# Kernel optimization log

Hardware: AMD Instinct MI355X
Metric: run time of the kernel (lower is better)

## Reference

```python
import jax, jax.numpy as jnp
import numpy as np


def setup_inputs() -> dict:
    key = jax.random.key(0)
    k1, k2, k3, k4 = jax.random.split(key, 4)
    B, S, d_in, d_out = 4, 2048, 1024, 1024
    x = jax.random.normal(k1, (B, S, d_in), dtype=jnp.float32)
    # torch nn.Linear weight is [d_out, d_in]; we store transposed [d_in, d_out]
    Wq = jax.random.normal(k2, (d_in, d_out), dtype=jnp.float32) * (1.0 / np.sqrt(d_in))
    Wk = jax.random.normal(k3, (d_in, d_out), dtype=jnp.float32) * (1.0 / np.sqrt(d_in))
    Wv = jax.random.normal(k4, (d_in, d_out), dtype=jnp.float32) * (1.0 / np.sqrt(d_in))
    return {"x": x, "Wq": Wq, "Wk": Wk, "Wv": Wv}


def reference(x, Wq, Wk, Wv):
    # x: [B, S, d_in]
    B, S, d_in = x.shape
    q = jnp.einsum("bsd,de->bse", x, Wq)
    k = jnp.einsum("bsd,de->bse", x, Wk)
    v = jnp.einsum("bsd,de->bse", x, Wv)
    scores = jnp.einsum("bqe,bke->bqk", q, k)  # [B, S, S]
    causal = jnp.triu(jnp.ones((S, S), dtype=bool), k=1)  # True above diagonal
    scores = jnp.where(causal[None, :, :], -jnp.inf, scores)
    # NOTE: original scales by sqrt(d_in), not sqrt(d_out)
    scale = jnp.asarray(1.0 / np.sqrt(d_in), dtype=scores.dtype)
    weights = jax.nn.softmax(scores * scale, axis=-1)
    # dropout p=0.0 -> identity
    return jnp.einsum("bqk,bke->bqe", weights, v)
```

## Files before the change

kernel.cpp:

```cpp
#include <hip/hip_runtime.h>
#include <hip/hip_bf16.h>

typedef __attribute__((ext_vector_type(8))) short short8;
typedef __attribute__((ext_vector_type(4))) float f32x4;
typedef unsigned short ushort_t;

__device__ __forceinline__ ushort_t f2bf(float f) {
    union { __hip_bfloat16 h; ushort_t u; } c;
    c.h = __float2bfloat16(f);
    return c.u;
}

__device__ __forceinline__ void gload16(const ushort_t* g, ushort_t* l) {
    __builtin_amdgcn_global_load_lds(
        (const __attribute__((address_space(1))) void*)g,
        (__attribute__((address_space(3))) void*)l, 16, 0, 0);
}

__global__ __launch_bounds__(256) void k_prep(const float* __restrict__ x,
                                              const float* __restrict__ W0,
                                              const float* __restrict__ W1,
                                              const float* __restrict__ W2,
                                              ushort_t* __restrict__ xb,
                                              ushort_t* __restrict__ Wt) {
    const int bz = blockIdx.z;
    if (bz == 3) {
        const int t = threadIdx.y * 32 + threadIdx.x;
        size_t base = ((size_t)(blockIdx.y * 32 + blockIdx.x) * 256 + t) * 8;
#pragma unroll
        for (int p = 0; p < 4; ++p) {
            size_t idx = base + (size_t)p * 2097152;
            float4 a = *(const float4*)(x + idx);
            float4 b = *(const float4*)(x + idx + 4);
            short8 o;
            o[0] = (short)f2bf(a.x); o[1] = (short)f2bf(a.y);
            o[2] = (short)f2bf(a.z); o[3] = (short)f2bf(a.w);
            o[4] = (short)f2bf(b.x); o[5] = (short)f2bf(b.y);
            o[6] = (short)f2bf(b.z); o[7] = (short)f2bf(b.w);
            *(short8*)(xb + idx) = o;
        }
        return;
    }
    const float* W = (bz == 0) ? W0 : (bz == 1) ? W1 : W2;
    ushort_t* out = Wt + (size_t)bz * 1024 * 1024;
    __shared__ float tile[32][33];
    int tx = threadIdx.x, ty = threadIdx.y;
    int d0 = blockIdx.y * 32, e0 = blockIdx.x * 32;
#pragma unroll
    for (int i = 0; i < 32; i += 8)
        tile[ty + i][tx] = W[(size_t)(d0 + ty + i) * 1024 + e0 + tx];
    __syncthreads();
#pragma unroll
    for (int i = 0; i < 32; i += 8)
        out[(size_t)(e0 + ty + i) * 1024 + d0 + tx] = f2bf(tile[tx][ty + i]);
}

template <int MODE>
__global__ __launch_bounds__(256) void k_gemm(const ushort_t* __restrict__ Abase,
                                              const ushort_t* __restrict__ Bbase,
                                              void* __restrict__ Cbase,
                                              ushort_t* __restrict__ Vt) {
    const int bz = blockIdx.z;
    int bm, bn;
    const ushort_t* A;
    const ushort_t* B;
    int lda, ldb, nk;
    if constexpr (MODE == 0) {
        bm = blockIdx.x; bn = blockIdx.y;
        A = Abase; lda = 1024;
        B = Bbase + (size_t)bz * 1024 * 1024; ldb = 1024;
        nk = 32;
    } else if constexpr (MODE == 1) {
        int x = blockIdx.x;
        bm = (int)((sqrtf(8.f * x + 1.f) - 1.f) * 0.5f);
        while ((bm + 1) * (bm + 2) / 2 <= x) ++bm;
        while (bm * (bm + 1) / 2 > x) --bm;
        bn = x - bm * (bm + 1) / 2;
        A = Abase + (size_t)bz * 2048 * 1024; lda = 1024;
        B = Bbase + (size_t)bz * 2048 * 1024; ldb = 1024;
        nk = 32;
    } else {
        int xr = blockIdx.x;
        bm = (xr & 1) ? (15 - (xr >> 1)) : (xr >> 1);
        bn = blockIdx.y;
        A = Abase + (size_t)bz * 2048 * 2048; lda = 2048;
        B = Bbase + (size_t)bz * 1024 * 2048; ldb = 2048;
        nk = (bm + 1) * 4;
    }

    constexpr int SMEM_ELEMS = (MODE == 0) ? (128 * 130) : 8192;
    __shared__ ushort_t smem[SMEM_ELEMS];
    ushort_t* As = smem;
    ushort_t* Bs = smem + 4096;

    const int tid = threadIdx.x;
    const int l = tid & 63, wid = tid >> 6;
    const int wr = (wid >> 1) * 64, wc = (wid & 1) * 64;
    const int lr = l & 15, kc = (l >> 4) * 8;

    const int srow = tid >> 2, skb = (tid & 3) * 8;
    const ushort_t* ag = A + (size_t)(bm * 128 + srow) * lda + skb;
    const ushort_t* bg = B + (size_t)(bn * 128 + srow) * ldb + skb;
    const size_t a64 = (size_t)64 * lda, b64 = (size_t)64 * ldb;
    ushort_t* al = As + tid * 8;
    ushort_t* bl = Bs + tid * 8;

    f32x4 zero = {0.f, 0.f, 0.f, 0.f};
    f32x4 acc[4][4];
#pragma unroll
    for (int m = 0; m < 4; ++m)
#pragma unroll
        for (int n = 0; n < 4; ++n) acc[m][n] = zero;

    f32x4 rs[4];
    short8 ones;
#pragma unroll
    for (int e = 0; e < 8; ++e) ones[e] = (short)0x3F80;
#pragma unroll
    for (int m = 0; m < 4; ++m) rs[m] = zero;

    for (int ks = 0; ks < nk; ++ks) {
        __syncthreads();
        gload16(ag, al);
        gload16(ag + a64, al + 2048);
        gload16(bg, bl);
        gload16(bg + b64, bl + 2048);
        ag += 32; bg += 32;
        __syncthreads();

        short8 a[4], b[4];
#pragma unroll
        for (int m = 0; m < 4; ++m)
            a[m] = *(const short8*)&As[(wr + m * 16 + lr) * 32 + kc];
#pragma unroll
        for (int n = 0; n < 4; ++n)
            b[n] = *(const short8*)&Bs[(wc + n * 16 + lr) * 32 + kc];
#pragma unroll
        for (int m = 0; m < 4; ++m)
#pragma unroll
            for (int n = 0; n < 4; ++n)
                acc[m][n] = __builtin_amdgcn_mfma_f32_16x16x32_bf16(a[m], b[n], acc[m][n], 0, 0, 0);
        if constexpr (MODE == 2) {
#pragma unroll
            for (int m = 0; m < 4; ++m)
                rs[m] = __builtin_amdgcn_mfma_f32_16x16x32_bf16(a[m], ones, rs[m], 0, 0, 0);
        }
    }

    const int rbase = (l >> 4) * 4;
    const int cbase = l & 15;

    if constexpr (MODE == 0) {
        if (bz == 2) {
            __syncthreads();
#pragma unroll
            for (int m = 0; m < 4; ++m)
#pragma unroll
                for (int n = 0; n < 4; ++n) {
                    int col = wc + n * 16 + cbase;
                    int row0 = wr + m * 16 + rbase;
#pragma unroll
                    for (int r = 0; r < 4; ++r)
                        smem[col * 130 + row0 + r] = f2bf(acc[m][n][r]);
                }
            __syncthreads();
            const int e = tid >> 1, jh = (tid & 1) * 64;
            const int b = bm >> 4, j0 = (bm * 128) & 2047;
            ushort_t* dst = Vt + (size_t)b * 2097152 +
                            (size_t)(bn * 128 + e) * 2048 + j0 + jh;
            const ushort_t* src = smem + e * 130 + jh;
#pragma unroll
            for (int c = 0; c < 8; ++c)
                *(short8*)(dst + c * 8) = *(const short8*)(src + c * 8);
            return;
        }
    }

    float inv[4][4];
    if constexpr (MODE == 2) {
#pragma unroll
        for (int m = 0; m < 4; ++m)
#pragma unroll
            for (int r = 0; r < 4; ++r) inv[m][r] = 1.0f / rs[m][r];
    }

#pragma unroll
    for (int m = 0; m < 4; ++m) {
#pragma unroll
        for (int n = 0; n < 4; ++n) {
            int row0 = wr + m * 16 + rbase;
            int col = wc + n * 16 + cbase;
            int gcol = bn * 128 + col;
#pragma unroll
            for (int r = 0; r < 4; ++r) {
                int grow = bm * 128 + row0 + r;
                float v = acc[m][n][r];
                if constexpr (MODE == 0) {
                    ushort_t* C = (ushort_t*)Cbase + (size_t)bz * 8192 * 1024;
                    C[(size_t)grow * 1024 + gcol] = f2bf(v);
                } else if constexpr (MODE == 1) {
                    ushort_t* C = (ushort_t*)Cbase + (size_t)bz * 2048 * 2048;
                    ushort_t pv = (gcol <= grow) ? f2bf(__expf(v * 0.03125f))
                                                 : (ushort_t)0;
                    C[(size_t)grow * 2048 + gcol] = pv;
                } else {
                    float* C = (float*)Cbase + (size_t)bz * 2048 * 1024;
                    C[(size_t)grow * 1024 + gcol] = v * inv[m][r];
                }
            }
        }
    }
}

extern "C" void kernel_launch(void* const* d_in, const int* in_sizes, int n_in,
                              void* d_out, int out_size, void* d_ws, size_t ws_size,
                              hipStream_t stream) {
    const float* x  = (const float*)d_in[0];
    const float* Wq = (const float*)d_in[1];
    const float* Wk = (const float*)d_in[2];
    const float* Wv = (const float*)d_in[3];

    char* ws = (char*)d_ws;
    ushort_t* xb     = (ushort_t*)(ws);
    ushort_t* Wt     = (ushort_t*)(ws + 16777216);
    ushort_t* QKV    = (ushort_t*)(ws + 23068672);
    ushort_t* Vt     = (ushort_t*)(ws + 73400320);
    ushort_t* P      = (ushort_t*)(ws + 90177536);

    ushort_t* Q = QKV;
    ushort_t* K = QKV + (size_t)8192 * 1024;

    k_prep<<<dim3(32, 32, 4), dim3(32, 8), 0, stream>>>(x, Wq, Wk, Wv, xb, Wt);
    k_gemm<0><<<dim3(64, 8, 3), 256, 0, stream>>>(xb, Wt, QKV, Vt);
    k_gemm<1><<<dim3(136, 1, 4), 256, 0, stream>>>(Q, K, P, nullptr);
    k_gemm<2><<<dim3(16, 8, 4), 256, 0, stream>>>(P, Vt, (float*)d_out, nullptr);
}
```

Baseline: 173.9 us.

## Fold Wq·Wk^T into one matrix so scores become x·M·x^T

Since q·k^T equals x·(Wq·Wk^T)·x^T, the change precomputes a 1024x1024 matrix M = Wk·Wq^T with a small GEMM. It then forms y = x·M and computes scores as y·x^T, instead of building separate Q and K projections. This drops one of the three large 8192x1024x1024 projection GEMMs in exchange for one 1024^3 GEMM. It also removes the K buffer and changes the weight prep to a plain cast for Wq and Wk. Rounding M and y to bf16 changes the numerical error profile slightly.

```diff
diff --git a/kernel.cpp b/kernel.cpp
--- a/kernel.cpp
+++ b/kernel.cpp
@@ -2,6 +2,7 @@
 #include <hip/hip_bf16.h>
 
 typedef __attribute__((ext_vector_type(8))) short short8;
+typedef __attribute__((ext_vector_type(4))) short short4_t;
 typedef __attribute__((ext_vector_type(4))) float f32x4;
 typedef unsigned short ushort_t;
 
@@ -18,14 +19,16 @@
 }
 
 __global__ __launch_bounds__(256) void k_prep(const float* __restrict__ x,
-                                              const float* __restrict__ W0,
-                                              const float* __restrict__ W1,
-                                              const float* __restrict__ W2,
+                                              const float* __restrict__ Wq,
+                                              const float* __restrict__ Wk,
+                                              const float* __restrict__ Wv,
                                               ushort_t* __restrict__ xb,
-                                              ushort_t* __restrict__ Wt) {
+                                              ushort_t* __restrict__ Wqb,
+                                              ushort_t* __restrict__ Wkb,
+                                              ushort_t* __restrict__ Wvt) {
     const int bz = blockIdx.z;
+    const int t = threadIdx.y * 32 + threadIdx.x;
     if (bz == 3) {
-        const int t = threadIdx.y * 32 + threadIdx.x;
         size_t base = ((size_t)(blockIdx.y * 32 + blockIdx.x) * 256 + t) * 8;
 #pragma unroll
         for (int p = 0; p < 4; ++p) {
@@ -41,18 +44,27 @@
         }
         return;
     }
-    const float* W = (bz == 0) ? W0 : (bz == 1) ? W1 : W2;
-    ushort_t* out = Wt + (size_t)bz * 1024 * 1024;
+    if (bz < 2) {
+        const float* src = bz ? Wk : Wq;
+        ushort_t* dst = bz ? Wkb : Wqb;
+        size_t idx = ((size_t)(blockIdx.y * 32 + blockIdx.x) * 256 + t) * 4;
+        float4 a = *(const float4*)(src + idx);
+        short4_t o;
+        o[0] = (short)f2bf(a.x); o[1] = (short)f2bf(a.y);
+        o[2] = (short)f2bf(a.z); o[3] = (short)f2bf(a.w);
+        *(short4_t*)(dst + idx) = o;
+        return;
+    }
     __shared__ float tile[32][33];
     int tx = threadIdx.x, ty = threadIdx.y;
     int d0 = blockIdx.y * 32, e0 = blockIdx.x * 32;
 #pragma unroll
     for (int i = 0; i < 32; i += 8)
-        tile[ty + i][tx] = W[(size_t)(d0 + ty + i) * 1024 + e0 + tx];
+        tile[ty + i][tx] = Wv[(size_t)(d0 + ty + i) * 1024 + e0 + tx];
     __syncthreads();
 #pragma unroll
     for (int i = 0; i < 32; i += 8)
-        out[(size_t)(e0 + ty + i) * 1024 + d0 + tx] = f2bf(tile[tx][ty + i]);
+        Wvt[(size_t)(e0 + ty + i) * 1024 + d0 + tx] = f2bf(tile[tx][ty + i]);
 }
 
 template <int MODE>
@@ -60,18 +72,22 @@
                                               const ushort_t* __restrict__ Bbase,
                                               void* __restrict__ Cbase,
                                               ushort_t* __restrict__ Vt) {
-    const int bz = blockIdx.z;
-    int bm, bn;
+    int bm, bn, bz;
     const ushort_t* A;
     const ushort_t* B;
     int lda, ldb, nk;
-    if constexpr (MODE == 0) {
-        bm = blockIdx.x; bn = blockIdx.y;
+    if constexpr (MODE == 3) {
+        bm = blockIdx.x; bn = blockIdx.y; bz = 0;
         A = Abase; lda = 1024;
-        B = Bbase + (size_t)bz * 1024 * 1024; ldb = 1024;
+        B = Bbase; ldb = 1024;
+        nk = 32;
+    } else if constexpr (MODE == 0) {
+        bm = blockIdx.x; bn = blockIdx.y; bz = blockIdx.z;
+        A = Abase; lda = 1024;
+        B = Bbase + (size_t)bz * 1048576; ldb = 1024;
         nk = 32;
     } else if constexpr (MODE == 1) {
-        int x = blockIdx.x;
+        int x = blockIdx.x; bz = blockIdx.z;
         bm = (int)((sqrtf(8.f * x + 1.f) - 1.f) * 0.5f);
         while ((bm + 1) * (bm + 2) / 2 <= x) ++bm;
         while (bm * (bm + 1) / 2 > x) --bm;
@@ -82,7 +98,7 @@
     } else {
         int xr = blockIdx.x;
         bm = (xr & 1) ? (15 - (xr >> 1)) : (xr >> 1);
-        bn = blockIdx.y;
+        bn = blockIdx.y; bz = blockIdx.z;
         A = Abase + (size_t)bz * 2048 * 2048; lda = 2048;
         B = Bbase + (size_t)bz * 1024 * 2048; ldb = 2048;
         nk = (bm + 1) * 4;
@@ -151,7 +167,7 @@
     const int cbase = l & 15;
 
     if constexpr (MODE == 0) {
-        if (bz == 2) {
+        if (bz == 1) {
             __syncthreads();
 #pragma unroll
             for (int m = 0; m < 4; ++m)
@@ -195,8 +211,8 @@
             for (int r = 0; r < 4; ++r) {
                 int grow = bm * 128 + row0 + r;
                 float v = acc[m][n][r];
-                if constexpr (MODE == 0) {
-                    ushort_t* C = (ushort_t*)Cbase + (size_t)bz * 8192 * 1024;
+                if constexpr (MODE == 0 || MODE == 3) {
+                    ushort_t* C = (ushort_t*)Cbase;
                     C[(size_t)grow * 1024 + gcol] = f2bf(v);
                 } else if constexpr (MODE == 1) {
                     ushort_t* C = (ushort_t*)Cbase + (size_t)bz * 2048 * 2048;
@@ -221,17 +237,18 @@
     const float* Wv = (const float*)d_in[3];
 
     char* ws = (char*)d_ws;
-    ushort_t* xb     = (ushort_t*)(ws);
-    ushort_t* Wt     = (ushort_t*)(ws + 16777216);
-    ushort_t* QKV    = (ushort_t*)(ws + 23068672);
-    ushort_t* Vt     = (ushort_t*)(ws + 73400320);
-    ushort_t* P      = (ushort_t*)(ws + 90177536);
-
-    ushort_t* Q = QKV;
-    ushort_t* K = QKV + (size_t)8192 * 1024;
-
-    k_prep<<<dim3(32, 32, 4), dim3(32, 8), 0, stream>>>(x, Wq, Wk, Wv, xb, Wt);
-    k_gemm<0><<<dim3(64, 8, 3), 256, 0, stream>>>(xb, Wt, QKV, Vt);
-    k_gemm<1><<<dim3(136, 1, 4), 256, 0, stream>>>(Q, K, P, nullptr);
+    ushort_t* xb  = (ushort_t*)(ws);
+    ushort_t* Wqb = (ushort_t*)(ws + 16777216);
+    ushort_t* Wkb = (ushort_t*)(ws + 18874368);
+    ushort_t* Mt  = (ushort_t*)(ws + 20971520);
+    ushort_t* Wvt = (ushort_t*)(ws + 23068672);
+    ushort_t* y   = (ushort_t*)(ws + 25165824);
+    ushort_t* Vt  = (ushort_t*)(ws + 41943040);
+    ushort_t* P   = (ushort_t*)(ws + 58720256);
+
+    k_prep<<<dim3(32, 32, 4), dim3(32, 8), 0, stream>>>(x, Wq, Wk, Wv, xb, Wqb, Wkb, Wvt);
+    k_gemm<3><<<dim3(8, 8), 256, 0, stream>>>(Wkb, Wqb, Mt, nullptr);
+    k_gemm<0><<<dim3(64, 8, 2), 256, 0, stream>>>(xb, Mt, y, Vt);
+    k_gemm<1><<<dim3(136, 1, 4), 256, 0, stream>>>(y, xb, P, nullptr);
     k_gemm<2><<<dim3(16, 8, 4), 256, 0, stream>>>(P, Vt, (float*)d_out, nullptr);
 }
```

Result: slower. 181.5 us (+4.4%).
